# Optimization experiments

Measured on AMD Instinct MI355X. Metric: run time of the kernel, lower is better.

## Reference

```python
import jax, jax.numpy as jnp
import numpy as np

B, T, N, F, H, R, E = 32, 8, 150, 16, 32, 4, 16


def _gconv(X, Af, Wf):
    # t-product graph conv (Kilmer t-product = circular conv over relation axis,
    # implemented facewise in the Fourier domain): ifft( fft(adj) @ fft(X) @ fft(W) )
    Xf = jnp.fft.fft(X, axis=-1)                      # [b,n,f,r] complex
    Y = jnp.einsum('nmr,bmfr->bnfr', Af, Xf)          # aggregate over nodes
    Y = jnp.einsum('bnfr,for->bnor', Y, Wf)           # feature transform
    return jnp.fft.ifft(Y, axis=-1).real


def _cell(X, Hs, Af, Wf, Bb):
    # TensorGRUCell. NOTE: faithful to the source, H_tilda reuses conv_hr
    # (conv_hh is defined but never used in the original forward).
    Wxz, Wxr, Wxh, Whz, Whr = Wf
    bz, br, bh = Bb[0], Bb[1], Bb[2]                  # [H,R], broadcasts over [b,n,H,R]
    Z = jax.nn.sigmoid(_gconv(X, Af, Wxz) + _gconv(Hs, Af, Whz) + bz)
    Rg = jax.nn.sigmoid(_gconv(X, Af, Wxr) + _gconv(Hs, Af, Whr) + br)
    Ht = jnp.tanh(_gconv(X, Af, Wxh) + _gconv(Rg * Hs, Af, Whr) + bh)
    return Z * Hs + (1.0 - Z) * Ht


def setup_inputs() -> dict:
    key = jax.random.key(0)
    ks = jax.random.split(key, 16)
    kai = lambda k, shp, fan: (jax.random.normal(k, shp, jnp.float32)
                               * np.float32(np.sqrt(2.0 / fan)))
    d = {}
    d['inputs'] = jax.random.normal(ks[0], (B, T, N, F, R), jnp.float32)
    d['U'] = kai(ks[1], (N, E, R), N)
    # layer 0 (input_dim=F)
    d['Wxz0'] = kai(ks[2], (F, H, R), F)
    d['Wxr0'] = kai(ks[3], (F, H, R), F)
    d['Wxh0'] = kai(ks[4], (F, H, R), F)
    d['Whz0'] = kai(ks[5], (H, H, R), H)
    d['Whr0'] = kai(ks[6], (H, H, R), H)
    d['B0'] = kai(ks[7], (3, H, R), 3)
    # layer 1 (input_dim=H)
    d['Wxz1'] = kai(ks[8], (H, H, R), H)
    d['Wxr1'] = kai(ks[9], (H, H, R), H)
    d['Wxh1'] = kai(ks[10], (H, H, R), H)
    d['Whz1'] = kai(ks[11], (H, H, R), H)
    d['Whr1'] = kai(ks[12], (H, H, R), H)
    d['B1'] = kai(ks[13], (3, H, R), 3)
    return d


def reference(inputs, U, Wxz0, Wxr0, Wxh0, Whz0, Whr0, B0,
              Wxz1, Wxr1, Wxh1, Whz1, Whr1, B1):
    # adaptive adjacency: softmax(relu(tprod(U, U^T)), dim=1)
    Uf = jnp.fft.fft(U, axis=-1)                      # [N,E,R] complex
    A = jnp.fft.ifft(jnp.einsum('ner,mer->nmr', Uf, Uf), axis=-1).real
    adj = jax.nn.softmax(jax.nn.relu(A), axis=1)      # [N,N,R]

    Af = jnp.fft.fft(adj, axis=-1)
    Wf0 = tuple(jnp.fft.fft(w, axis=-1) for w in (Wxz0, Wxr0, Wxh0, Whz0, Whr0))
    Wf1 = tuple(jnp.fft.fft(w, axis=-1) for w in (Wxz1, Wxr1, Wxh1, Whz1, Whr1))

    b, t, n, f, r = inputs.shape
    h = Whz0.shape[0]
    z0 = jnp.zeros((b, n, h, r), inputs.dtype)

    # t = 0: layer1 consumes the *current* layer0 output
    o0 = _cell(inputs[:, 0], z0, Af, Wf0, B0)
    o1 = _cell(o0, z0, Af, Wf1, B1)

    # t > 0: faithful to source, layer1 consumes the *previous timestep's*
    # layer0 output (temp_out[t-1][i-1]) with hidden temp_out[t-1][i].
    def step(carry, Xt):
        p0, p1 = carry
        n0 = _cell(Xt, p0, Af, Wf0, B0)
        n1 = _cell(p0, p1, Af, Wf1, B1)
        return (n0, n1), n1

    Xs = jnp.moveaxis(inputs[:, 1:], 1, 0)            # [T-1,B,N,F,R]
    (c0, c1), ys = jax.lax.scan(step, (o0, o1), Xs)

    out = jnp.concatenate([o1[None], ys], axis=0)     # [T,B,N,H,R]
    out = jnp.moveaxis(out, 0, 1)                     # [B,T,N,H,R]
    h_last = jnp.stack([c0, c1])                      # [L,B,N,H,R]
    return out, h_last
```

## Files before the change

### kernel.cpp

```cpp
#include <hip/hip_runtime.h>
#include <math.h>

#define NN 150
#define BB 32
#define TT 8
#define FF 16
#define HH 32
#define ROWS (NN*BB)
#define NCIN (BB*FF)
#define NCH  (BB*HH)
#define ADJ_LD 160

#define SZ_ADJF (4*NN*ADJ_LD)
#define SZ_WA0  (4*48*32*4)
#define SZ_WA1  (4*64*32*4)
#define SZ_WB   (32*32*4)
#define SZ_STATE (ROWS*HH*4)
#define SZ_PIN  (4*NN*NCIN)

__device__ __forceinline__ float sigmoidf_(float x){ return 1.f/(1.f+expf(-x)); }

__device__ __forceinline__ float comp_of4(float x0, float x1, float x2, float x3, int c) {
  return c==0 ? (x0+x1+x2+x3) : c==1 ? (x0-x2) : c==2 ? (x3-x1) : (x0-x1+x2-x3);
}


__global__ __launch_bounds__(256) void k_adj(const float* __restrict__ U, float* __restrict__ adjF) {
  __shared__ float Ufl[NN*16*4];
  __shared__ float Arow[NN*4];
  __shared__ float red[256];
  __shared__ float mxs[4], isms[4];
  int n = blockIdx.x, tid = threadIdx.x;
  for (int idx = tid; idx < NN*16; idx += 256) {
    const float* s = U + (size_t)idx*4;
    float x0=s[0], x1=s[1], x2=s[2], x3=s[3];
    Ufl[idx*4+0] = x0+x1+x2+x3;
    Ufl[idx*4+1] = x0-x2;
    Ufl[idx*4+2] = x3-x1;
    Ufl[idx*4+3] = x0-x1+x2-x3;
  }
  __syncthreads();
  if (tid < NN) {
    int m = tid;
    float a0=0, ar=0, ai=0, a2=0;
    #pragma unroll
    for (int e = 0; e < 16; ++e) {
      const float* un = &Ufl[(n*16+e)*4];
      const float* um = &Ufl[(m*16+e)*4];
      a0 += un[0]*um[0];
      ar += un[1]*um[1] - un[2]*um[2];
      ai += un[1]*um[2] + un[2]*um[1];
      a2 += un[3]*um[3];
    }
    float r0 = 0.25f*(a0 + 2.f*ar + a2);
    float r1 = 0.25f*(a0 - 2.f*ai - a2);
    float r2 = 0.25f*(a0 - 2.f*ar + a2);
    float r3 = 0.25f*(a0 + 2.f*ai - a2);
    Arow[m*4+0] = fmaxf(r0, 0.f);
    Arow[m*4+1] = fmaxf(r1, 0.f);
    Arow[m*4+2] = fmaxf(r2, 0.f);
    Arow[m*4+3] = fmaxf(r3, 0.f);
  }
  __syncthreads();
  for (int r = 0; r < 4; ++r) {
    float v = (tid < NN) ? Arow[tid*4+r] : -1e30f;
    red[tid] = v; __syncthreads();
    for (int s = 128; s > 0; s >>= 1) { if (tid < s) red[tid] = fmaxf(red[tid], red[tid+s]); __syncthreads(); }
    if (tid == 0) mxs[r] = red[0];
    __syncthreads();
    float e = (tid < NN) ? expf(Arow[tid*4+r] - mxs[r]) : 0.f;
    red[tid] = e; __syncthreads();
    for (int s = 128; s > 0; s >>= 1) { if (tid < s) red[tid] += red[tid+s]; __syncthreads(); }
    if (tid == 0) isms[r] = 1.f / red[0];
    __syncthreads();
    if (tid < NN) Arow[tid*4+r] = e * isms[r];
    __syncthreads();
  }
  if (tid < NN) {
    int m = tid;
    float e0=Arow[m*4+0], e1=Arow[m*4+1], e2=Arow[m*4+2], e3=Arow[m*4+3];
    size_t base = (size_t)n*ADJ_LD + m;
    size_t cs = (size_t)NN*ADJ_LD;
    adjF[base]      = e0+e1+e2+e3;
    adjF[base+cs]   = e0-e2;
    adjF[base+2*cs] = e3-e1;
    adjF[base+3*cs] = e0-e1+e2-e3;
  } else if (tid < ADJ_LD) {
    size_t base = (size_t)n*ADJ_LD + tid;
    size_t cs = (size_t)NN*ADJ_LD;
    adjF[base] = 0.f; adjF[base+cs] = 0.f; adjF[base+2*cs] = 0.f; adjF[base+3*cs] = 0.f;
  }
}

__global__ __launch_bounds__(256) void k_wts(
    const float* __restrict__ Wxz0, const float* __restrict__ Wxr0, const float* __restrict__ Wxh0,
    const float* __restrict__ Whz0, const float* __restrict__ Whr0,
    const float* __restrict__ Wxz1, const float* __restrict__ Wxr1, const float* __restrict__ Wxh1,
    const float* __restrict__ Whz1, const float* __restrict__ Whr1,
    float* __restrict__ WA0p, float* __restrict__ WA1p,
    float* __restrict__ WB0p, float* __restrict__ WB1p) {
  int idx = blockIdx.x*256 + threadIdx.x;
  const float* src = nullptr;
  float* dst; int didx; int c;
  if (idx < SZ_WA0) {
    c = idx / 6144;
    int rem = idx % 6144;
    int k = rem >> 7, og = (rem >> 2) & 31, q = rem & 3;
    if (q == 0) src = (k < FF) ? Wxz0 + ((size_t)k*HH + og)*4 : Whz0 + ((size_t)(k-FF)*HH + og)*4;
    else if (q == 1) src = (k < FF) ? Wxr0 + ((size_t)k*HH + og)*4 : Whr0 + ((size_t)(k-FF)*HH + og)*4;
    else if (q == 2 && k < FF) src = Wxh0 + ((size_t)k*HH + og)*4;
    dst = WA0p; didx = idx;
  } else if (idx < SZ_WA0 + SZ_WA1) {
    int id = idx - SZ_WA0;
    c = id >> 13;
    int rem = id & 8191;
    int k = rem >> 7, og = (rem >> 2) & 31, q = rem & 3;
    if (q == 0) src = (k < HH) ? Wxz1 + ((size_t)k*HH + og)*4 : Whz1 + ((size_t)(k-HH)*HH + og)*4;
    else if (q == 1) src = (k < HH) ? Wxr1 + ((size_t)k*HH + og)*4 : Whr1 + ((size_t)(k-HH)*HH + og)*4;
    else if (q == 2 && k < HH) src = Wxh1 + ((size_t)k*HH + og)*4;
    dst = WA1p; didx = id;
  } else if (idx < SZ_WA0 + SZ_WA1 + SZ_WB) {
    int id = idx - (SZ_WA0 + SZ_WA1);
    int k = id >> 7, o = (id >> 2) & 31;
    c = id & 3;
    src = Whr0 + ((size_t)k*HH + o)*4;
    dst = WB0p; didx = id;
  } else if (idx < SZ_WA0 + SZ_WA1 + 2*SZ_WB) {
    int id = idx - (SZ_WA0 + SZ_WA1 + SZ_WB);
    int k = id >> 7, o = (id >> 2) & 31;
    c = id & 3;
    src = Whr1 + ((size_t)k*HH + o)*4;
    dst = WB1p; didx = id;
  } else return;
  float v0=0,v1=0,v2=0,v3=0;
  if (src) { v0=src[0]; v1=src[1]; v2=src[2]; v3=src[3]; }
  dst[didx] = comp_of4(v0,v1,v2,v3,c);
}

struct AggParams {
  const float* X0; const float* X1; const float* X2;
  float* P0; float* P1; float* P2;
  int ncol0, ncol1, ncol2;
  int base1, base2, njobs, rawt, nb;
};
__global__ __launch_bounds__(256,4) void k_agg(AggParams pr, const float* __restrict__ adjF,
                                               const float* __restrict__ inp) {
  __shared__ float As[4*32*37];
  __shared__ float Xs[4*32*36];
  int bid = blockIdx.x;
  int part = (bid >= pr.nb) ? 1 : 0;
  if (part) bid -= pr.nb;
  const float* X; float* P; int ncol; int tile; bool raw = false;
  if (pr.njobs >= 3 && bid >= pr.base2) { X = pr.X2; P = pr.P2; ncol = pr.ncol2; tile = bid - pr.base2; }
  else if (pr.njobs >= 2 && bid >= pr.base1) { X = pr.X1; P = pr.P1; ncol = pr.ncol1; tile = bid - pr.base1; }
  else { X = pr.X0; P = pr.P0; ncol = pr.ncol0; tile = bid; raw = (pr.rawt >= 0); }
  P += (size_t)part * 4 * NN * ncol;
  int kbeg = part ? 96 : 0;
  int kend = part ? NN : 96;
  int n0 = (tile % 5) * 32;
  int col0 = (tile / 5) * 32;
  int tid = threadIdx.x;
  int ti = tid & 31, tj = tid >> 5;
  int j0 = tj * 4;
  float a0[4]={}, aR[4]={}, aI[4]={}, a2v[4]={};

  float4 pa[4];
  float4 px[4];

  #define LOAD_A(K0)                                                         \
    _Pragma("unroll")                                                        \
    for (int u = 0; u < 4; ++u) {                                            \
      int e = tid + u*256;                                                   \
      int c = e >> 8, rem = e & 255, i = rem >> 3, kq = rem & 7;             \
      int nn_ = n0 + i;                                                      \
      pa[u] = make_float4(0,0,0,0);                                          \
      if (nn_ < NN) pa[u] = *(const float4*)(adjF + ((size_t)c*NN + nn_)*ADJ_LD + (K0) + kq*4); \
    }
  #define STORE_A()                                                          \
    _Pragma("unroll")                                                        \
    for (int u = 0; u < 4; ++u) {                                            \
      int e = tid + u*256;                                                   \
      int c = e >> 8, rem = e & 255, i = rem >> 3, kq = rem & 7;             \
      As[(c*32 + kq*4+0)*37 + i] = pa[u].x;                                  \
      As[(c*32 + kq*4+1)*37 + i] = pa[u].y;                                  \
      As[(c*32 + kq*4+2)*37 + i] = pa[u].z;                                  \
      As[(c*32 + kq*4+3)*37 + i] = pa[u].w;                                  \
    }
  #define LOAD_X(K0)                                                         \
    if (raw) {                                                               \
      int q = tid & 7, kk = tid >> 3;                                        \
      int mm = (K0) + kk;                                                    \
      int col = col0 + q*4;                                                  \
      int b = col >> 4, f = col & 15;                                        \
      px[0]=px[1]=px[2]=px[3]=make_float4(0,0,0,0);                          \
      if (mm < NN) {                                                         \
        const float* s = inp + (((size_t)(b*TT + pr.rawt)*NN + mm)*FF + f)*4;\
        px[0] = *(const float4*)(s+0);                                       \
        px[1] = *(const float4*)(s+4);                                       \
        px[2] = *(const float4*)(s+8);                                       \
        px[3] = *(const float4*)(s+12);                                      \
      }                                                                      \
    } else {                                                                 \
      _Pragma("unroll")                                                      \
      for (int u = 0; u < 4; ++u) {                                          \
        int e = tid + u*256;                                                 \
        int c = e >> 8, rem = e & 255, kk = rem >> 3, q = rem & 7;           \
        int mm = (K0) + kk;                                                  \
        px[u] = make_float4(0,0,0,0);                                        \
        if (mm < NN) px[u] = *(const float4*)(X + ((size_t)c*NN + mm)*ncol + col0 + q*4); \
      }                                                                      \
    }
  #define STORE_X()                                                          \
    if (raw) {                                                               \
      int q = tid & 7, kk = tid >> 3;                                        \
      float4 r0 = px[0], r1 = px[1], r2 = px[2], r3 = px[3];                 \
      float4 w;                                                              \
      w = make_float4(r0.x+r0.y+r0.z+r0.w, r1.x+r1.y+r1.z+r1.w, r2.x+r2.y+r2.z+r2.w, r3.x+r3.y+r3.z+r3.w); \
      *(float4*)&Xs[(0*32+kk)*36 + q*4] = w;                                 \
      w = make_float4(r0.x-r0.z, r1.x-r1.z, r2.x-r2.z, r3.x-r3.z);           \
      *(float4*)&Xs[(1*32+kk)*36 + q*4] = w;                                 \
      w = make_float4(r0.w-r0.y, r1.w-r1.y, r2.w-r2.y, r3.w-r3.y);           \
      *(float4*)&Xs[(2*32+kk)*36 + q*4] = w;                                 \
      w = make_float4(r0.x-r0.y+r0.z-r0.w, r1.x-r1.y+r1.z-r1.w, r2.x-r2.y+r2.z-r2.w, r3.x-r3.y+r3.z-r3.w); \
      *(float4*)&Xs[(3*32+kk)*36 + q*4] = w;                                 \
    } else {                                                                 \
      _Pragma("unroll")                                                      \
      for (int u = 0; u < 4; ++u) {                                          \
        int e = tid + u*256;                                                 \
        int c = e >> 8, rem = e & 255, kk = rem >> 3, q = rem & 7;           \
        *(float4*)&Xs[(c*32+kk)*36 + q*4] = px[u];                           \
      }                                                                      \
    }

  LOAD_A(kbeg)
  LOAD_X(kbeg)
  for (int k0 = kbeg; k0 < kend; k0 += 32) {
    STORE_A()
    STORE_X()
    __syncthreads();
    int k0n = k0 + 32;
    if (k0n < kend) {
      LOAD_A(k0n)
      LOAD_X(k0n)
    }
    #pragma unroll 4
    for (int k = 0; k < 32; ++k) {
      float A0 = As[(0*32+k)*37 + ti];
      float A1 = As[(1*32+k)*37 + ti];
      float A2 = As[(2*32+k)*37 + ti];
      float A3 = As[(3*32+k)*37 + ti];
      float4 x0 = *(float4*)&Xs[(0*32+k)*36 + j0];
      float4 x1 = *(float4*)&Xs[(1*32+k)*36 + j0];
      float4 x2 = *(float4*)&Xs[(2*32+k)*36 + j0];
      float4 x3 = *(float4*)&Xs[(3*32+k)*36 + j0];
      float X0v[4]={x0.x,x0.y,x0.z,x0.w}, X1v[4]={x1.x,x1.y,x1.z,x1.w};
      float X2v[4]={x2.x,x2.y,x2.z,x2.w}, X3v[4]={x3.x,x3.y,x3.z,x3.w};
      #pragma unroll
      for (int j = 0; j < 4; ++j) {
        a0[j] += A0*X0v[j];
        aR[j] += A1*X1v[j] - A2*X2v[j];
        aI[j] += A1*X2v[j] + A2*X1v[j];
        a2v[j] += A3*X3v[j];
      }
    }
    __syncthreads();
  }
  int nn_ = n0 + ti;
  if (nn_ < NN) {
    size_t cs = (size_t)NN*ncol;
    size_t rb = (size_t)nn_*ncol + col0 + j0;
    *(float4*)&P[rb]      = make_float4(a0[0],a0[1],a0[2],a0[3]);
    *(float4*)&P[rb+cs]   = make_float4(aR[0],aR[1],aR[2],aR[3]);
    *(float4*)&P[rb+2*cs] = make_float4(aI[0],aI[1],aI[2],aI[3]);
    *(float4*)&P[rb+3*cs] = make_float4(a2v[0],a2v[1],a2v[2],a2v[3]);
  }
}

struct FAJob {
  const float* Px;
  const float* Ph;
  const float* W;
  const float* bias;
  const float* hprev;
  float* Z; float* T1; float* Mf;
  int zh;
};
struct FAParams { FAJob j[2]; };

template<int KTOT, int KX>
__device__ __forceinline__ void fusedA_body(const FAJob& jb, float* Ps) {
  int row0 = blockIdx.x * 8;
  int tid = threadIdx.x;
  int r = tid >> 5, og = tid & 31;
  int row = row0 + r;
  const size_t psx = (size_t)4*ROWS*KX;
  const size_t psh = (size_t)4*ROWS*HH;
  for (int kk = og; kk < KTOT; kk += 32) {
    #pragma unroll
    for (int c = 0; c < 4; ++c) {
      float v;
      if (kk < KX) {
        size_t ix = ((size_t)c*ROWS + row)*KX + kk;
        v = jb.Px[ix] + jb.Px[ix + psx];
      } else {
        if (jb.zh) v = 0.f;
        else {
          size_t ih = ((size_t)c*ROWS + row)*HH + (kk-KX);
          v = jb.Ph[ih] + jb.Ph[ih + psh];
        }
      }
      Ps[(r*KTOT + kk)*4 + c] = v;
    }
  }
  __syncthreads();
  float acc0[3]={}, accR[3]={}, accI[3]={}, acc2[3]={};
  const float* W = jb.W;
  #pragma unroll 4
  for (int k = 0; k < KTOT; ++k) {
    float4 p  = *(const float4*)&Ps[(r*KTOT + k)*4];
    float4 w0 = *(const float4*)&W[((size_t)(0*KTOT + k)*32 + og)*4];
    float4 w1 = *(const float4*)&W[((size_t)(1*KTOT + k)*32 + og)*4];
    float4 w2 = *(const float4*)&W[((size_t)(2*KTOT + k)*32 + og)*4];
    float4 w3 = *(const float4*)&W[((size_t)(3*KTOT + k)*32 + og)*4];
    float W0v[3]={w0.x,w0.y,w0.z}, W1v[3]={w1.x,w1.y,w1.z};
    float W2v[3]={w2.x,w2.y,w2.z}, W3v[3]={w3.x,w3.y,w3.z};
    #pragma unroll
    for (int q = 0; q < 3; ++q) {
      acc0[q] += p.x*W0v[q];
      accR[q] += p.y*W1v[q] - p.z*W2v[q];
      accI[q] += p.y*W2v[q] + p.z*W1v[q];
      acc2[q] += p.w*W3v[q];
    }
  }
  float ys[3][4];
  #pragma unroll
  for (int q = 0; q < 3; ++q) {
    float Y0 = acc0[q], Yr = accR[q], Yi = accI[q], Y2 = acc2[q];
    ys[q][0] = 0.25f*(Y0 + 2.f*Yr + Y2);
    ys[q][1] = 0.25f*(Y0 - 2.f*Yi - Y2);
    ys[q][2] = 0.25f*(Y0 - 2.f*Yr + Y2);
    ys[q][3] = 0.25f*(Y0 + 2.f*Yi - Y2);
  }
  {
    const float* bz = jb.bias + (0*HH + og)*4;
    float4 z = make_float4(sigmoidf_(ys[0][0]+bz[0]), sigmoidf_(ys[0][1]+bz[1]),
                           sigmoidf_(ys[0][2]+bz[2]), sigmoidf_(ys[0][3]+bz[3]));
    *(float4*)&jb.Z[((size_t)row*HH + og)*4] = z;
  }
  {
    const float* br = jb.bias + (1*HH + og)*4;
    float4 hp = make_float4(0,0,0,0);
    if (!jb.zh) hp = *(const float4*)&jb.hprev[((size_t)row*HH + og)*4];
    float m0 = sigmoidf_(ys[1][0]+br[0]) * hp.x;
    float m1 = sigmoidf_(ys[1][1]+br[1]) * hp.y;
    float m2 = sigmoidf_(ys[1][2]+br[2]) * hp.z;
    float m3 = sigmoidf_(ys[1][3]+br[3]) * hp.w;
    size_t mb = (size_t)row*HH + og;
    size_t cs = (size_t)ROWS*HH;
    jb.Mf[mb]      = m0+m1+m2+m3;
    jb.Mf[mb+cs]   = m0-m2;
    jb.Mf[mb+2*cs] = m3-m1;
    jb.Mf[mb+3*cs] = m0-m1+m2-m3;
  }
  {
    const float* bh = jb.bias + (2*HH + og)*4;
    float4 tv = make_float4(ys[2][0]+bh[0], ys[2][1]+bh[1], ys[2][2]+bh[2], ys[2][3]+bh[3]);
    *(float4*)&jb.T1[((size_t)row*HH + og)*4] = tv;
  }
}

__global__ __launch_bounds__(256,4) void k_fusedA_both(FAParams pr) {
  __shared__ float Ps[8*64*4];
  if (blockIdx.y == 0) fusedA_body<48,16>(pr.j[0], Ps);
  else                 fusedA_body<64,32>(pr.j[1], Ps);
}
__global__ __launch_bounds__(256,4) void k_fusedA_L0(FAParams pr) {
  __shared__ float Ps[8*48*4];
  fusedA_body<48,16>(pr.j[0], Ps);
}
__global__ __launch_bounds__(256,4) void k_fusedA_L1(FAParams pr) {
  __shared__ float Ps[8*64*4];
  fusedA_body<64,32>(pr.j[1], Ps);
}

struct FBJob {
  const float* Pm; const float* W; const float* T1; const float* Z;
  float* h; float* hf; float* outp; float* hlast;
  int t, zh, wout;
};
struct FBParams { FBJob j[2]; };
__global__ __launch_bounds__(256,4) void k_fusedB(FBParams pr) {
  __shared__ float Ps[8*32*4];
  FBJob jb = pr.j[blockIdx.y];
  int row0 = blockIdx.x * 8;
  int tid = threadIdx.x;
  int r = tid >> 5, o = tid & 31;
  int row = row0 + r;
  float acc0=0, accR=0, accI=0, acc2=0;
  if (!jb.zh) {
    const size_t psh = (size_t)4*ROWS*HH;
    #pragma unroll
    for (int c = 0; c < 4; ++c) {
      size_t ix = ((size_t)c*ROWS + row)*HH + o;
      Ps[(r*32 + o)*4 + c] = jb.Pm[ix] + jb.Pm[ix + psh];
    }
    __syncthreads();
    #pragma unroll 8
    for (int k = 0; k < 32; ++k) {
      float4 p = *(const float4*)&Ps[(r*32 + k)*4];
      float4 w = *(const float4*)&jb.W[((size_t)(k*32 + o))*4];
      acc0 += p.x*w.x;
      accR += p.y*w.y - p.z*w.z;
      accI += p.y*w.z + p.z*w.y;
      acc2 += p.w*w.w;
    }
  }
  float y0 = 0.25f*(acc0 + 2.f*accR + acc2);
  float y1 = 0.25f*(acc0 - 2.f*accI - acc2);
  float y2 = 0.25f*(acc0 - 2.f*accR + acc2);
  float y3 = 0.25f*(acc0 + 2.f*accI - acc2);
  float4 t1 = *(const float4*)&jb.T1[((size_t)row*HH + o)*4];
  float h0v = tanhf(t1.x + y0);
  float h1v = tanhf(t1.y + y1);
  float h2v = tanhf(t1.z + y2);
  float h3v = tanhf(t1.w + y3);
  float4 z = *(const float4*)&jb.Z[((size_t)row*HH + o)*4];
  float4 hp = make_float4(0,0,0,0);
  if (!jb.zh) hp = *(const float4*)&jb.h[((size_t)row*HH + o)*4];
  float n0v = z.x*hp.x + (1.f-z.x)*h0v;
  float n1v = z.y*hp.y + (1.f-z.y)*h1v;
  float n2v = z.z*hp.z + (1.f-z.z)*h2v;
  float n3v = z.w*hp.w + (1.f-z.w)*h3v;
  *(float4*)&jb.h[((size_t)row*HH + o)*4] = make_float4(n0v,n1v,n2v,n3v);
  size_t hb = (size_t)row*HH + o, cs = (size_t)ROWS*HH;
  jb.hf[hb]      = n0v+n1v+n2v+n3v;
  jb.hf[hb+cs]   = n0v-n2v;
  jb.hf[hb+2*cs] = n3v-n1v;
  jb.hf[hb+3*cs] = n0v-n1v+n2v-n3v;
  int n = row >> 5, b = row & 31;
  if (jb.wout) {
    float* dst = jb.outp + (((size_t)b*TT + jb.t)*NN + n)*(HH*4) + o*4;
    *(float4*)dst = make_float4(n0v,n1v,n2v,n3v);
  }
  if (jb.hlast) {
    float* dst = jb.hlast + ((size_t)(b*NN + n))*(HH*4) + o*4;
    *(float4*)dst = make_float4(n0v,n1v,n2v,n3v);
  }
}

extern "C" void kernel_launch(void* const* d_in, const int* in_sizes, int n_in,
                              void* d_out, int out_size, void* d_ws, size_t ws_size,
                              hipStream_t stream) {
  const float* inp  = (const float*)d_in[0];
  const float* U    = (const float*)d_in[1];
  const float* Wxz0 = (const float*)d_in[2];
  const float* Wxr0 = (const float*)d_in[3];
  const float* Wxh0 = (const float*)d_in[4];
  const float* Whz0 = (const float*)d_in[5];
  const float* Whr0 = (const float*)d_in[6];
  const float* B0   = (const float*)d_in[7];
  const float* Wxz1 = (const float*)d_in[8];
  const float* Wxr1 = (const float*)d_in[9];
  const float* Wxh1 = (const float*)d_in[10];
  const float* Whz1 = (const float*)d_in[11];
  const float* Whr1 = (const float*)d_in[12];
  const float* B1   = (const float*)d_in[13];
  float* out = (float*)d_out;

  float* ws = (float*)d_ws;
  float* ADJF = ws;  ws += SZ_ADJF;
  float* WA0  = ws;  ws += SZ_WA0;
  float* WA1  = ws;  ws += SZ_WA1;
  float* WB0  = ws;  ws += SZ_WB;
  float* WB1  = ws;  ws += SZ_WB;
  float* H0   = ws;  ws += SZ_STATE;
  float* H1   = ws;  ws += SZ_STATE;
  float* H0F  = ws;  ws += SZ_STATE;
  float* H1F  = ws;  ws += SZ_STATE;
  float* PIN  = ws;  ws += 2*SZ_PIN;
  float* PH0  = ws;  ws += 2*SZ_STATE;
  float* PH1  = ws;  ws += 2*SZ_STATE;
  float* PM0  = ws;  ws += 2*SZ_STATE;
  float* PM1  = ws;  ws += 2*SZ_STATE;
  float* M0F  = ws;  ws += SZ_STATE;
  float* M1F  = ws;  ws += SZ_STATE;
  float* Z0   = ws;  ws += SZ_STATE;
  float* Z1   = ws;  ws += SZ_STATE;
  float* T10  = ws;  ws += SZ_STATE;
  float* T11  = ws;  ws += SZ_STATE;

  k_adj<<<NN, 256, 0, stream>>>(U, ADJF);
  k_wts<<<(SZ_WA0+SZ_WA1+2*SZ_WB+255)/256, 256, 0, stream>>>(
      Wxz0,Wxr0,Wxh0,Whz0,Whr0,Wxz1,Wxr1,Wxh1,Whz1,Whr1,WA0,WA1,WB0,WB1);

  {
    AggParams p; p.X0=nullptr; p.P0=PIN; p.ncol0=NCIN;
    p.X1=nullptr; p.P1=nullptr; p.ncol1=0; p.X2=nullptr; p.P2=nullptr; p.ncol2=0;
    p.base1=0; p.base2=0; p.njobs=1; p.rawt=0; p.nb=80;
    k_agg<<<160, 256, 0, stream>>>(p, ADJF, inp);
  }
  {
    FAParams p;
    p.j[0] = FAJob{PIN, nullptr, WA0, B0, nullptr, Z0, T10, M0F, 1};
    p.j[1] = p.j[0];
    k_fusedA_L0<<<dim3(600,1), 256, 0, stream>>>(p);
  }
  {
    FBParams p;
    p.j[0] = FBJob{nullptr, WB0, T10, Z0, H0, H0F, nullptr, nullptr, 0, 1, 0};
    p.j[1] = p.j[0];
    k_fusedB<<<dim3(600,1), 256, 0, stream>>>(p);
  }
  {
    AggParams p; p.X0=H0F; p.P0=PH0; p.ncol0=NCH;
    p.X1=nullptr; p.P1=nullptr; p.ncol1=0; p.X2=nullptr; p.P2=nullptr; p.ncol2=0;
    p.base1=0; p.base2=0; p.njobs=1; p.rawt=-1; p.nb=160;
    k_agg<<<320, 256, 0, stream>>>(p, ADJF, inp);
  }
  {
    FAParams p;
    p.j[0] = FAJob{PH0, nullptr, WA1, B1, nullptr, Z1, T11, M1F, 1};
    p.j[1] = p.j[0];
    k_fusedA_L1<<<dim3(600,1), 256, 0, stream>>>(p);
  }
  {
    FBParams p;
    p.j[0] = FBJob{nullptr, WB1, T11, Z1, H1, H1F, out, nullptr, 0, 1, 1};
    p.j[1] = p.j[0];
    k_fusedB<<<dim3(600,1), 256, 0, stream>>>(p);
  }

  float* hlast0 = out + (size_t)BB*TT*NN*HH*4;
  float* hlast1 = hlast0 + (size_t)BB*NN*HH*4;
  for (int t = 1; t < TT; ++t) {
    {
      AggParams p;
      p.X0=nullptr; p.P0=PIN; p.ncol0=NCIN;
      p.X1=H0F; p.P1=PH0; p.ncol1=NCH;
      p.X2=H1F; p.P2=PH1; p.ncol2=NCH;
      p.base1=80; p.base2=240; p.njobs=3; p.rawt=t; p.nb=400;
      k_agg<<<800, 256, 0, stream>>>(p, ADJF, inp);
    }
    {
      FAParams p;
      p.j[0] = FAJob{PIN, PH0, WA0, B0, H0, Z0, T10, M0F, 0};
      p.j[1] = FAJob{PH0, PH1, WA1, B1, H1, Z1, T11, M1F, 0};
      k_fusedA_both<<<dim3(600,2), 256, 0, stream>>>(p);
    }
    {
      AggParams p;
      p.X0=M0F; p.P0=PM0; p.ncol0=NCH;
      p.X1=M1F; p.P1=PM1; p.ncol1=NCH;
      p.X2=nullptr; p.P2=nullptr; p.ncol2=0;
      p.base1=160; p.base2=0; p.njobs=2; p.rawt=-1; p.nb=320;
      k_agg<<<640, 256, 0, stream>>>(p, ADJF, inp);
    }
    {
      int last = (t == TT-1);
      FBParams p;
      p.j[0] = FBJob{PM0, WB0, T10, Z0, H0, H0F, nullptr, last ? hlast0 : nullptr, t, 0, 0};
      p.j[1] = FBJob{PM1, WB1, T11, Z1, H1, H1F, out,     last ? hlast1 : nullptr, t, 0, 1};
      k_fusedB<<<dim3(600,2), 256, 0, stream>>>(p);
    }
  }
}
```

Baseline: 884.5 us.

## Stage weights in shared memory and compute two rows per thread in fused gate kernels

The fused gate kernels (A and B) now handle 16 rows per block instead of 8, and each thread accumulates two rows, so every weight value is used twice. Weights are staged into shared memory in K-chunks instead of being read per thread from global memory, and the P tile is loaded with float4 vector reads into a padded planar layout. The aim is less global weight traffic and better arithmetic reuse. In exchange the grid is halved to 300 blocks per job, and occupancy drops (launch bounds 3 for kernel A) because of the larger shared-memory footprint and extra accumulator registers.

```diff
diff --git a/kernel.cpp b/kernel.cpp
--- a/kernel.cpp
+++ b/kernel.cpp
@@ -10,6 +10,7 @@
 #define NCIN (BB*FF)
 #define NCH  (BB*HH)
 #define ADJ_LD 160
+#define KPAD 68
 
 #define SZ_ADJF (4*NN*ADJ_LD)
 #define SZ_WA0  (4*48*32*4)
@@ -288,99 +289,132 @@
 struct FAParams { FAJob j[2]; };
 
 template<int KTOT, int KX>
-__device__ __forceinline__ void fusedA_body(const FAJob& jb, float* Ps) {
-  int row0 = blockIdx.x * 8;
-  int tid = threadIdx.x;
-  int r = tid >> 5, og = tid & 31;
-  int row = row0 + r;
+__device__ __forceinline__ void fusedA_body(const FAJob& jb, float* Ps, float* Ws) {
+  const int row0 = blockIdx.x * 16;
+  const int tid = threadIdx.x;
+  const int og = tid & 31;
+  const int rg = tid >> 5;
+  const int r0 = rg*2, r1 = rg*2 + 1;
   const size_t psx = (size_t)4*ROWS*KX;
   const size_t psh = (size_t)4*ROWS*HH;
-  for (int kk = og; kk < KTOT; kk += 32) {
+  constexpr int K4 = KTOT/4;
+  for (int e = tid; e < 16*4*K4; e += 256) {
+    int k4 = e % K4; int c = (e / K4) & 3; int r = e / (K4*4);
+    int k = k4*4;
+    int row = row0 + r;
+    float4 v;
+    if (k < KX) {
+      const float* a = &jb.Px[((size_t)c*ROWS + row)*KX + k];
+      float4 va = *(const float4*)a;
+      float4 vb = *(const float4*)(a + psx);
+      v = make_float4(va.x+vb.x, va.y+vb.y, va.z+vb.z, va.w+vb.w);
+    } else if (jb.zh) {
+      v = make_float4(0,0,0,0);
+    } else {
+      const float* a = &jb.Ph[((size_t)c*ROWS + row)*HH + (k - KX)];
+      float4 va = *(const float4*)a;
+      float4 vb = *(const float4*)(a + psh);
+      v = make_float4(va.x+vb.x, va.y+vb.y, va.z+vb.z, va.w+vb.w);
+    }
+    *(float4*)&Ps[(r*4 + c)*KPAD + k] = v;
+  }
+  float acc0[2][3]={{0,0,0},{0,0,0}}, accR[2][3]={{0,0,0},{0,0,0}};
+  float accI[2][3]={{0,0,0},{0,0,0}}, acc2[2][3]={{0,0,0},{0,0,0}};
+  constexpr int NCHK = KTOT/16;
+  const float4* Wg = (const float4*)jb.W;
+  for (int cc = 0; cc < NCHK; ++cc) {
+    __syncthreads();
     #pragma unroll
-    for (int c = 0; c < 4; ++c) {
-      float v;
-      if (kk < KX) {
-        size_t ix = ((size_t)c*ROWS + row)*KX + kk;
-        v = jb.Px[ix] + jb.Px[ix + psx];
-      } else {
-        if (jb.zh) v = 0.f;
-        else {
-          size_t ih = ((size_t)c*ROWS + row)*HH + (kk-KX);
-          v = jb.Ph[ih] + jb.Ph[ih + psh];
-        }
+    for (int u = 0; u < 8; ++u) {
+      int f = tid + u*256;
+      int c = f >> 9, rem = f & 511;
+      float4 v = Wg[((size_t)c*KTOT + cc*16)*32 + rem];
+      *(float4*)&Ws[((size_t)c*512 + rem)*4] = v;
+    }
+    __syncthreads();
+    #pragma unroll 4
+    for (int kk = 0; kk < 16; ++kk) {
+      int k = cc*16 + kk;
+      float p0a = Ps[(r0*4+0)*KPAD + k];
+      float p1a = Ps[(r0*4+1)*KPAD + k];
+      float p2a = Ps[(r0*4+2)*KPAD + k];
+      float p3a = Ps[(r0*4+3)*KPAD + k];
+      float p0b = Ps[(r1*4+0)*KPAD + k];
+      float p1b = Ps[(r1*4+1)*KPAD + k];
+      float p2b = Ps[(r1*4+2)*KPAD + k];
+      float p3b = Ps[(r1*4+3)*KPAD + k];
+      float4 w0 = *(float4*)&Ws[((0*16+kk)*32+og)*4];
+      float4 w1 = *(float4*)&Ws[((1*16+kk)*32+og)*4];
+      float4 w2 = *(float4*)&Ws[((2*16+kk)*32+og)*4];
+      float4 w3 = *(float4*)&Ws[((3*16+kk)*32+og)*4];
+      float W0v[3]={w0.x,w0.y,w0.z}, W1v[3]={w1.x,w1.y,w1.z};
+      float W2v[3]={w2.x,w2.y,w2.z}, W3v[3]={w3.x,w3.y,w3.z};
+      #pragma unroll
+      for (int q = 0; q < 3; ++q) {
+        acc0[0][q] += p0a*W0v[q];
+        acc0[1][q] += p0b*W0v[q];
+        accR[0][q] += p1a*W1v[q] - p2a*W2v[q];
+        accR[1][q] += p1b*W1v[q] - p2b*W2v[q];
+        accI[0][q] += p1a*W2v[q] + p2a*W1v[q];
+        accI[1][q] += p1b*W2v[q] + p2b*W1v[q];
+        acc2[0][q] += p3a*W3v[q];
+        acc2[1][q] += p3b*W3v[q];
       }
-      Ps[(r*KTOT + kk)*4 + c] = v;
-    }
-  }
-  __syncthreads();
-  float acc0[3]={}, accR[3]={}, accI[3]={}, acc2[3]={};
-  const float* W = jb.W;
-  #pragma unroll 4
-  for (int k = 0; k < KTOT; ++k) {
-    float4 p  = *(const float4*)&Ps[(r*KTOT + k)*4];
-    float4 w0 = *(const float4*)&W[((size_t)(0*KTOT + k)*32 + og)*4];
-    float4 w1 = *(const float4*)&W[((size_t)(1*KTOT + k)*32 + og)*4];
-    float4 w2 = *(const float4*)&W[((size_t)(2*KTOT + k)*32 + og)*4];
-    float4 w3 = *(const float4*)&W[((size_t)(3*KTOT + k)*32 + og)*4];
-    float W0v[3]={w0.x,w0.y,w0.z}, W1v[3]={w1.x,w1.y,w1.z};
-    float W2v[3]={w2.x,w2.y,w2.z}, W3v[3]={w3.x,w3.y,w3.z};
+    }
+  }
+  const float* bz = jb.bias + (0*HH + og)*4;
+  const float* br = jb.bias + (1*HH + og)*4;
+  const float* bh = jb.bias + (2*HH + og)*4;
+  float bzv[4] = {bz[0],bz[1],bz[2],bz[3]};
+  float brv[4] = {br[0],br[1],br[2],br[3]};
+  float bhv[4] = {bh[0],bh[1],bh[2],bh[3]};
+  #pragma unroll
+  for (int rr = 0; rr < 2; ++rr) {
+    int row = row0 + rg*2 + rr;
+    float ys[3][4];
     #pragma unroll
     for (int q = 0; q < 3; ++q) {
-      acc0[q] += p.x*W0v[q];
-      accR[q] += p.y*W1v[q] - p.z*W2v[q];
-      accI[q] += p.y*W2v[q] + p.z*W1v[q];
-      acc2[q] += p.w*W3v[q];
-    }
-  }
-  float ys[3][4];
-  #pragma unroll
-  for (int q = 0; q < 3; ++q) {
-    float Y0 = acc0[q], Yr = accR[q], Yi = accI[q], Y2 = acc2[q];
-    ys[q][0] = 0.25f*(Y0 + 2.f*Yr + Y2);
-    ys[q][1] = 0.25f*(Y0 - 2.f*Yi - Y2);
-    ys[q][2] = 0.25f*(Y0 - 2.f*Yr + Y2);
-    ys[q][3] = 0.25f*(Y0 + 2.f*Yi - Y2);
-  }
-  {
-    const float* bz = jb.bias + (0*HH + og)*4;
-    float4 z = make_float4(sigmoidf_(ys[0][0]+bz[0]), sigmoidf_(ys[0][1]+bz[1]),
-                           sigmoidf_(ys[0][2]+bz[2]), sigmoidf_(ys[0][3]+bz[3]));
+      float Y0 = acc0[rr][q], Yr = accR[rr][q], Yi = accI[rr][q], Y2 = acc2[rr][q];
+      ys[q][0] = 0.25f*(Y0 + 2.f*Yr + Y2);
+      ys[q][1] = 0.25f*(Y0 - 2.f*Yi - Y2);
+      ys[q][2] = 0.25f*(Y0 - 2.f*Yr + Y2);
+      ys[q][3] = 0.25f*(Y0 + 2.f*Yi - Y2);
+    }
+    float4 z = make_float4(sigmoidf_(ys[0][0]+bzv[0]), sigmoidf_(ys[0][1]+bzv[1]),
+                           sigmoidf_(ys[0][2]+bzv[2]), sigmoidf_(ys[0][3]+bzv[3]));
     *(float4*)&jb.Z[((size_t)row*HH + og)*4] = z;
-  }
-  {
-    const float* br = jb.bias + (1*HH + og)*4;
     float4 hp = make_float4(0,0,0,0);
     if (!jb.zh) hp = *(const float4*)&jb.hprev[((size_t)row*HH + og)*4];
-    float m0 = sigmoidf_(ys[1][0]+br[0]) * hp.x;
-    float m1 = sigmoidf_(ys[1][1]+br[1]) * hp.y;
-    float m2 = sigmoidf_(ys[1][2]+br[2]) * hp.z;
-    float m3 = sigmoidf_(ys[1][3]+br[3]) * hp.w;
+    float m0 = sigmoidf_(ys[1][0]+brv[0]) * hp.x;
+    float m1 = sigmoidf_(ys[1][1]+brv[1]) * hp.y;
+    float m2 = sigmoidf_(ys[1][2]+brv[2]) * hp.z;
+    float m3 = sigmoidf_(ys[1][3]+brv[3]) * hp.w;
     size_t mb = (size_t)row*HH + og;
     size_t cs = (size_t)ROWS*HH;
     jb.Mf[mb]      = m0+m1+m2+m3;
     jb.Mf[mb+cs]   = m0-m2;
     jb.Mf[mb+2*cs] = m3-m1;
     jb.Mf[mb+3*cs] = m0-m1+m2-m3;
-  }
-  {
-    const float* bh = jb.bias + (2*HH + og)*4;
-    float4 tv = make_float4(ys[2][0]+bh[0], ys[2][1]+bh[1], ys[2][2]+bh[2], ys[2][3]+bh[3]);
+    float4 tv = make_float4(ys[2][0]+bhv[0], ys[2][1]+bhv[1], ys[2][2]+bhv[2], ys[2][3]+bhv[3]);
     *(float4*)&jb.T1[((size_t)row*HH + og)*4] = tv;
   }
 }
 
-__global__ __launch_bounds__(256,4) void k_fusedA_both(FAParams pr) {
-  __shared__ float Ps[8*64*4];
-  if (blockIdx.y == 0) fusedA_body<48,16>(pr.j[0], Ps);
-  else                 fusedA_body<64,32>(pr.j[1], Ps);
-}
-__global__ __launch_bounds__(256,4) void k_fusedA_L0(FAParams pr) {
-  __shared__ float Ps[8*48*4];
-  fusedA_body<48,16>(pr.j[0], Ps);
-}
-__global__ __launch_bounds__(256,4) void k_fusedA_L1(FAParams pr) {
-  __shared__ float Ps[8*64*4];
-  fusedA_body<64,32>(pr.j[1], Ps);
+__global__ __launch_bounds__(256,3) void k_fusedA_both(FAParams pr) {
+  __shared__ float Ps[16*4*KPAD];
+  __shared__ float Ws[8192];
+  if (blockIdx.y == 0) fusedA_body<48,16>(pr.j[0], Ps, Ws);
+  else                 fusedA_body<64,32>(pr.j[1], Ps, Ws);
+}
+__global__ __launch_bounds__(256,3) void k_fusedA_L0(FAParams pr) {
+  __shared__ float Ps[16*4*KPAD];
+  __shared__ float Ws[8192];
+  fusedA_body<48,16>(pr.j[0], Ps, Ws);
+}
+__global__ __launch_bounds__(256,3) void k_fusedA_L1(FAParams pr) {
+  __shared__ float Ps[16*4*KPAD];
+  __shared__ float Ws[8192];
+  fusedA_body<64,32>(pr.j[1], Ps, Ws);
 }
 
 struct FBJob {
@@ -390,61 +424,81 @@
 };
 struct FBParams { FBJob j[2]; };
 __global__ __launch_bounds__(256,4) void k_fusedB(FBParams pr) {
-  __shared__ float Ps[8*32*4];
+  __shared__ float Ps[16*32*4];
+  __shared__ float Ws[32*32*4];
   FBJob jb = pr.j[blockIdx.y];
-  int row0 = blockIdx.x * 8;
+  int row0 = blockIdx.x * 16;
   int tid = threadIdx.x;
-  int r = tid >> 5, o = tid & 31;
-  int row = row0 + r;
-  float acc0=0, accR=0, accI=0, acc2=0;
+  int rg = tid >> 5, o = tid & 31;
+  int r0 = rg*2, r1 = r0 + 1;
+  float acc0[2]={0,0}, accR[2]={0,0}, accI[2]={0,0}, acc2[2]={0,0};
   if (!jb.zh) {
+    #pragma unroll
+    for (int u = 0; u < 4; ++u) {
+      int f = tid + u*256;
+      ((float4*)Ws)[f] = ((const float4*)jb.W)[f];
+    }
     const size_t psh = (size_t)4*ROWS*HH;
     #pragma unroll
-    for (int c = 0; c < 4; ++c) {
-      size_t ix = ((size_t)c*ROWS + row)*HH + o;
-      Ps[(r*32 + o)*4 + c] = jb.Pm[ix] + jb.Pm[ix + psh];
+    for (int u = 0; u < 2; ++u) {
+      int e = tid + u*256;
+      int r = e >> 5, k = e & 31;
+      int row = row0 + r;
+      float4 v;
+      float* vv = (float*)&v;
+      #pragma unroll
+      for (int c = 0; c < 4; ++c) {
+        size_t ix = ((size_t)c*ROWS + row)*HH + k;
+        vv[c] = jb.Pm[ix] + jb.Pm[ix + psh];
+      }
+      *(float4*)&Ps[(r*32 + k)*4] = v;
     }
     __syncthreads();
     #pragma unroll 8
     for (int k = 0; k < 32; ++k) {
-      float4 p = *(const float4*)&Ps[(r*32 + k)*4];
-      float4 w = *(const float4*)&jb.W[((size_t)(k*32 + o))*4];
-      acc0 += p.x*w.x;
-      accR += p.y*w.y - p.z*w.z;
-      accI += p.y*w.z + p.z*w.y;
-      acc2 += p.w*w.w;
-    }
-  }
-  float y0 = 0.25f*(acc0 + 2.f*accR + acc2);
-  float y1 = 0.25f*(acc0 - 2.f*accI - acc2);
-  float y2 = 0.25f*(acc0 - 2.f*accR + acc2);
-  float y3 = 0.25f*(acc0 + 2.f*accI - acc2);
-  float4 t1 = *(const float4*)&jb.T1[((size_t)row*HH + o)*4];
-  float h0v = tanhf(t1.x + y0);
-  float h1v = tanhf(t1.y + y1);
-  float h2v = tanhf(t1.z + y2);
-  float h3v = tanhf(t1.w + y3);
-  float4 z = *(const float4*)&jb.Z[((size_t)row*HH + o)*4];
-  float4 hp = make_float4(0,0,0,0);
-  if (!jb.zh) hp = *(const float4*)&jb.h[((size_t)row*HH + o)*4];
-  float n0v = z.x*hp.x + (1.f-z.x)*h0v;
-  float n1v = z.y*hp.y + (1.f-z.y)*h1v;
-  float n2v = z.z*hp.z + (1.f-z.z)*h2v;
-  float n3v = z.w*hp.w + (1.f-z.w)*h3v;
-  *(float4*)&jb.h[((size_t)row*HH + o)*4] = make_float4(n0v,n1v,n2v,n3v);
-  size_t hb = (size_t)row*HH + o, cs = (size_t)ROWS*HH;
-  jb.hf[hb]      = n0v+n1v+n2v+n3v;
-  jb.hf[hb+cs]   = n0v-n2v;
-  jb.hf[hb+2*cs] = n3v-n1v;
-  jb.hf[hb+3*cs] = n0v-n1v+n2v-n3v;
-  int n = row >> 5, b = row & 31;
-  if (jb.wout) {
-    float* dst = jb.outp + (((size_t)b*TT + jb.t)*NN + n)*(HH*4) + o*4;
-    *(float4*)dst = make_float4(n0v,n1v,n2v,n3v);
-  }
-  if (jb.hlast) {
-    float* dst = jb.hlast + ((size_t)(b*NN + n))*(HH*4) + o*4;
-    *(float4*)dst = make_float4(n0v,n1v,n2v,n3v);
+      float4 pA = *(const float4*)&Ps[(r0*32 + k)*4];
+      float4 pB = *(const float4*)&Ps[(r1*32 + k)*4];
+      float4 w  = *(const float4*)&Ws[(k*32 + o)*4];
+      acc0[0] += pA.x*w.x;  acc0[1] += pB.x*w.x;
+      accR[0] += pA.y*w.y - pA.z*w.z;  accR[1] += pB.y*w.y - pB.z*w.z;
+      accI[0] += pA.y*w.z + pA.z*w.y;  accI[1] += pB.y*w.z + pB.z*w.y;
+      acc2[0] += pA.w*w.w;  acc2[1] += pB.w*w.w;
+    }
+  }
+  #pragma unroll
+  for (int rr = 0; rr < 2; ++rr) {
+    int row = row0 + rg*2 + rr;
+    float y0 = 0.25f*(acc0[rr] + 2.f*accR[rr] + acc2[rr]);
+    float y1 = 0.25f*(acc0[rr] - 2.f*accI[rr] - acc2[rr]);
+    float y2 = 0.25f*(acc0[rr] - 2.f*accR[rr] + acc2[rr]);
+    float y3 = 0.25f*(acc0[rr] + 2.f*accI[rr] - acc2[rr]);
+    float4 t1 = *(const float4*)&jb.T1[((size_t)row*HH + o)*4];
+    float h0v = tanhf(t1.x + y0);
+    float h1v = tanhf(t1.y + y1);
+    float h2v = tanhf(t1.z + y2);
+    float h3v = tanhf(t1.w + y3);
+    float4 z = *(const float4*)&jb.Z[((size_t)row*HH + o)*4];
+    float4 hp = make_float4(0,0,0,0);
+    if (!jb.zh) hp = *(const float4*)&jb.h[((size_t)row*HH + o)*4];
+    float n0v = z.x*hp.x + (1.f-z.x)*h0v;
+    float n1v = z.y*hp.y + (1.f-z.y)*h1v;
+    float n2v = z.z*hp.z + (1.f-z.z)*h2v;
+    float n3v = z.w*hp.w + (1.f-z.w)*h3v;
+    *(float4*)&jb.h[((size_t)row*HH + o)*4] = make_float4(n0v,n1v,n2v,n3v);
+    size_t hb = (size_t)row*HH + o, cs = (size_t)ROWS*HH;
+    jb.hf[hb]      = n0v+n1v+n2v+n3v;
+    jb.hf[hb+cs]   = n0v-n2v;
+    jb.hf[hb+2*cs] = n3v-n1v;
+    jb.hf[hb+3*cs] = n0v-n1v+n2v-n3v;
+    int n = row >> 5, b = row & 31;
+    if (jb.wout) {
+      float* dst = jb.outp + (((size_t)b*TT + jb.t)*NN + n)*(HH*4) + o*4;
+      *(float4*)dst = make_float4(n0v,n1v,n2v,n3v);
+    }
+    if (jb.hlast) {
+      float* dst = jb.hlast + ((size_t)(b*NN + n))*(HH*4) + o*4;
+      *(float4*)dst = make_float4(n0v,n1v,n2v,n3v);
+    }
   }
 }
 
@@ -503,13 +557,13 @@
     FAParams p;
     p.j[0] = FAJob{PIN, nullptr, WA0, B0, nullptr, Z0, T10, M0F, 1};
     p.j[1] = p.j[0];
-    k_fusedA_L0<<<dim3(600,1), 256, 0, stream>>>(p);
+    k_fusedA_L0<<<dim3(300,1), 256, 0, stream>>>(p);
   }
   {
     FBParams p;
     p.j[0] = FBJob{nullptr, WB0, T10, Z0, H0, H0F, nullptr, nullptr, 0, 1, 0};
     p.j[1] = p.j[0];
-    k_fusedB<<<dim3(600,1), 256, 0, stream>>>(p);
+    k_fusedB<<<dim3(300,1), 256, 0, stream>>>(p);
   }
   {
     AggParams p; p.X0=H0F; p.P0=PH0; p.ncol0=NCH;
@@ -521,13 +575,13 @@
     FAParams p;
     p.j[0] = FAJob{PH0, nullptr, WA1, B1, nullptr, Z1, T11, M1F, 1};
     p.j[1] = p.j[0];
-    k_fusedA_L1<<<dim3(600,1), 256, 0, stream>>>(p);
+    k_fusedA_L1<<<dim3(300,1), 256, 0, stream>>>(p);
   }
   {
     FBParams p;
     p.j[0] = FBJob{nullptr, WB1, T11, Z1, H1, H1F, out, nullptr, 0, 1, 1};
     p.j[1] = p.j[0];
-    k_fusedB<<<dim3(600,1), 256, 0, stream>>>(p);
+    k_fusedB<<<dim3(300,1), 256, 0, stream>>>(p);
   }
 
   float* hlast0 = out + (size_t)BB*TT*NN*HH*4;
@@ -545,7 +599,7 @@
       FAParams p;
       p.j[0] = FAJob{PIN, PH0, WA0, B0, H0, Z0, T10, M0F, 0};
       p.j[1] = FAJob{PH0, PH1, WA1, B1, H1, Z1, T11, M1F, 0};
-      k_fusedA_both<<<dim3(600,2), 256, 0, stream>>>(p);
+      k_fusedA_both<<<dim3(300,2), 256, 0, stream>>>(p);
     }
     {
       AggParams p;
@@ -560,7 +614,7 @@
       FBParams p;
       p.j[0] = FBJob{PM0, WB0, T10, Z0, H0, H0F, nullptr, last ? hlast0 : nullptr, t, 0, 0};
       p.j[1] = FBJob{PM1, WB1, T11, Z1, H1, H1F, out,     last ? hlast1 : nullptr, t, 0, 1};
-      k_fusedB<<<dim3(600,2), 256, 0, stream>>>(p);
-    }
-  }
-}
+      k_fusedB<<<dim3(300,2), 256, 0, stream>>>(p);
+    }
+  }
+}
```

New measurement: 846.2 us. 1.05x faster.
